# Performance work log

Measured on AMD Instinct MI355X. Metric: run time of the kernel, lower is better.

The kernel has to match this reference:

```python
import jax, jax.numpy as jnp
import numpy as np

N = 200_000   # nodes
E = 6_400_000 # edges (avg degree 32)


def setup_inputs() -> dict:
    key = jax.random.key(0)
    k = jax.random.split(key, 6)
    x = jax.random.normal(k[0], (N, 2), dtype=jnp.float32)
    edge_index = jax.random.randint(k[1], (2, E), 0, N, dtype=jnp.int32)
    # GCNConv(2, 8) and GCNConv(8, 4) parameters (Glorot-ish init, zero bias as in PyG)
    W1 = jax.random.normal(k[2], (2, 8), dtype=jnp.float32) * (1.0 / np.sqrt(2.0))
    b1 = jnp.zeros((8,), dtype=jnp.float32)
    W2 = jax.random.normal(k[3], (8, 4), dtype=jnp.float32) * (1.0 / np.sqrt(8.0))
    b2 = jnp.zeros((4,), dtype=jnp.float32)
    return {"x": x, "edge_index": edge_index, "W1": W1, "b1": b1, "W2": W2, "b2": b2}


def _gcn_conv(x, src, dst, norm, W, b, n):
    # PyG GCNConv: linear transform, normalized gather/scatter-add, bias after aggregation
    h = x @ W                                   # [N, F_out]
    msg = h[src] * norm[:, None]                # gather + edge-wise scale, [E', F_out]
    agg = jax.ops.segment_sum(msg, dst, num_segments=n)  # scatter-add at targets
    return agg + b


def reference(x, edge_index, W1, b1, W2, b2):
    n = x.shape[0]
    # add self-loops (PyG default add_self_loops=True)
    loops = jnp.arange(n, dtype=edge_index.dtype)
    src = jnp.concatenate([edge_index[0], loops])
    dst = jnp.concatenate([edge_index[1], loops])
    # symmetric degree normalization: deg computed at targets with unit edge weights
    deg = jax.ops.segment_sum(jnp.ones_like(src, dtype=x.dtype), dst, num_segments=n)
    deg_inv_sqrt = jnp.where(deg > 0, jax.lax.rsqrt(jnp.maximum(deg, 1.0)), 0.0)
    norm = deg_inv_sqrt[src] * deg_inv_sqrt[dst]  # [E']

    h = jax.nn.relu(_gcn_conv(x, src, dst, norm, W1, b1, n))
    out = _gcn_conv(h, src, dst, norm, W2, b2, n)
    return out
```

## Files before the change

kernel.cpp:

```cpp
#include <hip/hip_runtime.h>


#define EPB   8192
#define PART  2048
#define LPBIT 11
#define SRCB  18
#define BC    4
#define RSTR  2049
#define CAP   70656
#define STCAP 17664


__global__ __launch_bounds__(512) void sortA_kernel(
    const int* __restrict__ src, const int* __restrict__ dst,
    int* __restrict__ cursor, unsigned* __restrict__ packed, int E, int P) {
    __shared__ int cnt[128];
    int tid = threadIdx.x;
    if (tid < 128) cnt[tid] = 0;
    __syncthreads();
    int nv4 = E >> 2;
    int b4 = (blockIdx.x * EPB) >> 2;
    int e4 = min(b4 + (EPB >> 2), nv4);
    const int4* d4 = (const int4*)dst;
    const int4* s4 = (const int4*)src;
    #pragma unroll
    for (int k = 0; k < (EPB >> 2); k += 512) {
        int i = b4 + k + tid;
        if (i < e4) {
            int4 d = d4[i];
            atomicAdd(&cnt[d.x >> LPBIT], 1);
            atomicAdd(&cnt[d.y >> LPBIT], 1);
            atomicAdd(&cnt[d.z >> LPBIT], 1);
            atomicAdd(&cnt[d.w >> LPBIT], 1);
        }
    }
    bool lastblk = (blockIdx.x == gridDim.x - 1);
    if (lastblk) {
        int e = (nv4 << 2) + tid;
        if (e < E) atomicAdd(&cnt[dst[e] >> LPBIT], 1);
    }
    __syncthreads();
    if (tid < P) {
        int c = cnt[tid];
        int base = (c > 0) ? atomicAdd(&cursor[tid], c) : 0;
        cnt[tid] = tid * CAP + base;
    }
    __syncthreads();
    #pragma unroll
    for (int k = 0; k < (EPB >> 2); k += 512) {
        int i = b4 + k + tid;
        if (i < e4) {
            int4 d = d4[i];
            int4 sv = s4[i];
            int p0 = atomicAdd(&cnt[d.x >> LPBIT], 1);
            packed[p0] = ((unsigned)(d.x & (PART - 1)) << SRCB) | (unsigned)sv.x;
            int p1 = atomicAdd(&cnt[d.y >> LPBIT], 1);
            packed[p1] = ((unsigned)(d.y & (PART - 1)) << SRCB) | (unsigned)sv.y;
            int p2 = atomicAdd(&cnt[d.z >> LPBIT], 1);
            packed[p2] = ((unsigned)(d.z & (PART - 1)) << SRCB) | (unsigned)sv.z;
            int p3 = atomicAdd(&cnt[d.w >> LPBIT], 1);
            packed[p3] = ((unsigned)(d.w & (PART - 1)) << SRCB) | (unsigned)sv.w;
        }
    }
    if (lastblk) {
        int e = (nv4 << 2) + tid;
        if (e < E) {
            int d = dst[e];
            int pos = atomicAdd(&cnt[d >> LPBIT], 1);
            packed[pos] = ((unsigned)(d & (PART - 1)) << SRCB) | (unsigned)src[e];
        }
    }
}


__global__ __launch_bounds__(512) void localC_kernel(
    const unsigned* __restrict__ packed, const int* __restrict__ cursor,
    int* __restrict__ runStart, int* __restrict__ srcsorted) {
    __shared__ int hist[PART];
    __shared__ int sdata[512];
    __shared__ unsigned stage[STCAP];
    int tid = threadIdx.x;
    int dp = blockIdx.x >> 2, b = blockIdx.x & (BC - 1);
    int dpbase = dp * CAP;
    int tot = cursor[dp];
    int lo = dpbase + (int)(((long long)tot * b) / BC);
    int hi = dpbase + (int)(((long long)tot * (b + 1)) / BC);
    for (int k = tid; k < PART; k += 512) hist[k] = 0;
    __syncthreads();
    for (int i = lo + tid; i < hi; i += 512)
        atomicAdd(&hist[packed[i] >> SRCB], 1);
    __syncthreads();
    int off = tid * 4;
    int v0 = hist[off], v1 = hist[off + 1], v2 = hist[off + 2], v3 = hist[off + 3];
    int s = v0 + v1 + v2 + v3;
    int x = s;
    sdata[tid] = x;
    __syncthreads();
    for (int o = 1; o < 512; o <<= 1) {
        int t = (tid >= o) ? sdata[tid - o] : 0;
        __syncthreads();
        x += t;
        sdata[tid] = x;
        __syncthreads();
    }
    int run = x - s;
    int* rs = runStart + (size_t)(dp * BC + b) * RSTR;
    int c0 = lo + run, c1 = c0 + v0, c2 = c1 + v1, c3 = c2 + v2;
    rs[off] = c0; rs[off + 1] = c1; rs[off + 2] = c2; rs[off + 3] = c3;
    __syncthreads();
    hist[off] = c0; hist[off + 1] = c1; hist[off + 2] = c2; hist[off + 3] = c3;
    if (tid == 0) rs[PART] = hi;
    __syncthreads();
    int total = hi - lo;
    bool ovf = total > STCAP;
    for (int i = lo + tid; i < hi; i += 512) {
        unsigned w = packed[i];
        int pos = atomicAdd(&hist[w >> SRCB], 1);
        unsigned sv = w & ((1u << SRCB) - 1);
        if (!ovf) stage[pos - lo] = sv;
        else srcsorted[pos] = sv;
    }
    __syncthreads();
    if (!ovf)
        for (int j = tid; j < total; j += 512) srcsorted[lo + j] = (int)stage[j];
}


__global__ __launch_bounds__(512) void dinvg_kernel(
    const int* __restrict__ runStart, const float* __restrict__ x,
    float* __restrict__ dinv, float* __restrict__ g, int n) {
    int i = blockIdx.x * 512 + threadIdx.x;
    if (i >= n) return;
    int dp = i >> LPBIT, ld = i & (PART - 1);
    int deg = 0;
    #pragma unroll
    for (int b = 0; b < BC; b++) {
        const int* rs = runStart + (size_t)(dp * BC + b) * RSTR + ld;
        deg += rs[1] - rs[0];
    }
    float d = rsqrtf((float)deg + 1.0f);
    dinv[i] = d;
    float2 xv = ((const float2*)x)[i];
    ((float2*)g)[i] = make_float2(xv.x * d, xv.y * d);
}

__global__ __launch_bounds__(512) void agg1_kernel(
    const int* __restrict__ runStart, const int* __restrict__ srcsorted,
    const float* __restrict__ g, const float* __restrict__ dinv,
    const float* __restrict__ W1, const float* __restrict__ b1,
    const float* __restrict__ W2, float* __restrict__ hs2, int n) {
    int t = blockIdx.x * 512 + threadIdx.x;
    int i = t >> 2, b = t & 3;
    bool valid = i < n;
    const float2* gp = (const float2*)g;
    float s0 = 0.0f, s1 = 0.0f;
    if (valid) {
        int dp = i >> LPBIT, ld = i & (PART - 1);
        const int* rs = runStart + (size_t)(dp * BC + b) * RSTR + ld;
        int p0 = rs[0], p1 = rs[1];
        int p = p0;
        for (; p + 4 <= p1; p += 4) {
            int a = srcsorted[p], bb = srcsorted[p + 1];
            int c = srcsorted[p + 2], e = srcsorted[p + 3];
            float2 w0 = gp[a], w1 = gp[bb], w2 = gp[c], w3 = gp[e];
            s0 += w0.x + w1.x + w2.x + w3.x;
            s1 += w0.y + w1.y + w2.y + w3.y;
        }
        for (; p < p1; p++) {
            float2 w = gp[srcsorted[p]];
            s0 += w.x;
            s1 += w.y;
        }
    }
    s0 += __shfl_xor(s0, 1); s1 += __shfl_xor(s1, 1);
    s0 += __shfl_xor(s0, 2); s1 += __shfl_xor(s1, 2);
    if (valid && b == 0) {
        float d = dinv[i];
        float2 gi = gp[i];
        s0 = (s0 + gi.x) * d;
        s1 = (s1 + gi.y) * d;
        float h[8];
        #pragma unroll
        for (int f = 0; f < 8; f++)
            h[f] = fmaxf(s0 * W1[f] + s1 * W1[8 + f] + b1[f], 0.0f);
        float oc[4];
        #pragma unroll
        for (int k = 0; k < 4; k++) {
            float a = 0.0f;
            #pragma unroll
            for (int f = 0; f < 8; f++) a += h[f] * W2[4 * f + k];
            oc[k] = a * d;
        }
        float4 o;
        o.x = oc[0]; o.y = oc[1]; o.z = oc[2]; o.w = oc[3];
        *(float4*)(hs2 + 4 * (size_t)i) = o;
    }
}

__global__ __launch_bounds__(512) void agg2_kernel(
    const int* __restrict__ runStart, const int* __restrict__ srcsorted,
    const float* __restrict__ hs2, const float* __restrict__ dinv,
    const float* __restrict__ b2, float* __restrict__ out, int n) {
    int t = blockIdx.x * 512 + threadIdx.x;
    int i = t >> 2, b = t & 3;
    bool valid = i < n;
    const float4* hp = (const float4*)hs2;
    float s0 = 0.0f, s1 = 0.0f, s2 = 0.0f, s3 = 0.0f;
    if (valid) {
        int dp = i >> LPBIT, ld = i & (PART - 1);
        const int* rs = runStart + (size_t)(dp * BC + b) * RSTR + ld;
        int p0 = rs[0], p1 = rs[1];
        int p = p0;
        for (; p + 4 <= p1; p += 4) {
            int a = srcsorted[p], bb = srcsorted[p + 1];
            int c = srcsorted[p + 2], e = srcsorted[p + 3];
            float4 w0 = hp[a], w1 = hp[bb], w2 = hp[c], w3 = hp[e];
            s0 += w0.x + w1.x + w2.x + w3.x;
            s1 += w0.y + w1.y + w2.y + w3.y;
            s2 += w0.z + w1.z + w2.z + w3.z;
            s3 += w0.w + w1.w + w2.w + w3.w;
        }
        for (; p < p1; p++) {
            float4 w = hp[srcsorted[p]];
            s0 += w.x; s1 += w.y; s2 += w.z; s3 += w.w;
        }
    }
    s0 += __shfl_xor(s0, 1); s1 += __shfl_xor(s1, 1);
    s2 += __shfl_xor(s2, 1); s3 += __shfl_xor(s3, 1);
    s0 += __shfl_xor(s0, 2); s1 += __shfl_xor(s1, 2);
    s2 += __shfl_xor(s2, 2); s3 += __shfl_xor(s3, 2);
    if (valid && b == 0) {
        float d = dinv[i];
        float4 hi2 = hp[i];
        float4 o;
        o.x = d * (s0 + hi2.x) + b2[0];
        o.y = d * (s1 + hi2.y) + b2[1];
        o.z = d * (s2 + hi2.z) + b2[2];
        o.w = d * (s3 + hi2.w) + b2[3];
        *(float4*)(out + 4 * (size_t)i) = o;
    }
}

extern "C" void kernel_launch(void* const* d_in, const int* in_sizes, int n_in,
                              void* d_out, int out_size, void* d_ws, size_t ws_size,
                              hipStream_t stream) {
    const float* x   = (const float*)d_in[0];
    const int*   ei  = (const int*)d_in[1];
    const float* W1  = (const float*)d_in[2];
    const float* b1  = (const float*)d_in[3];
    const float* W2  = (const float*)d_in[4];
    const float* b2  = (const float*)d_in[5];
    float* out = (float*)d_out;

    const int n = in_sizes[0] / 2;
    const int E = in_sizes[1] / 2;
    const int* src = ei;
    const int* dst = ei + E;

    const int P  = (n + PART - 1) >> LPBIT;
    const int B1 = (E + EPB - 1) / EPB;

    int* ws = (int*)d_ws;
    int* cursor = ws;
    int* runStart = ws + 128;
    size_t rssz = (((size_t)P * BC * RSTR) + 3) & ~(size_t)3;
    unsigned* packed = (unsigned*)(runStart + rssz);
    int* srcsorted = (int*)(packed + (size_t)P * CAP);
    size_t nd = (size_t)P << LPBIT;
    float* dinv = (float*)packed;
    float* g    = dinv + nd;
    float* hs2  = g + 2 * nd;

    hipMemsetAsync(cursor, 0, 128 * sizeof(int), stream);

    const int gN  = (n + 511) / 512;
    const int gN4 = (4 * n + 511) / 512;

    sortA_kernel <<<B1, 512, 0, stream>>>(src, dst, cursor, packed, E, P);
    localC_kernel<<<P * BC, 512, 0, stream>>>(packed, cursor, runStart, srcsorted);
    dinvg_kernel <<<gN, 512, 0, stream>>>(runStart, x, dinv, g, n);
    agg1_kernel  <<<gN4, 512, 0, stream>>>(runStart, srcsorted, g, dinv, W1, b1, W2, hs2, n);
    agg2_kernel  <<<gN4, 512, 0, stream>>>(runStart, srcsorted, hs2, dinv, b2, out, n);
}
```

Before: 252.5 us.

## Use per-wave partition counters in sort and split each node's edges over eight lanes

```diff
diff --git a/kernel.cpp b/kernel.cpp
--- a/kernel.cpp
+++ b/kernel.cpp
@@ -5,60 +5,70 @@
 #define PART  2048
 #define LPBIT 11
 #define SRCB  18
-#define BC    4
+#define BC    8
 #define RSTR  2049
-#define CAP   70656
-#define STCAP 17664
+#define CAP   69632
+#define STCAP 8704
+#define WV    8
 
 
 __global__ __launch_bounds__(512) void sortA_kernel(
     const int* __restrict__ src, const int* __restrict__ dst,
     int* __restrict__ cursor, unsigned* __restrict__ packed, int E, int P) {
-    __shared__ int cnt[128];
+    __shared__ int cnt[WV * 128];
+    __shared__ int wcur[WV * 128];
     int tid = threadIdx.x;
-    if (tid < 128) cnt[tid] = 0;
+    int wid = tid >> 6;
+    for (int k = tid; k < WV * 128; k += 512) cnt[k] = 0;
     __syncthreads();
     int nv4 = E >> 2;
     int b4 = (blockIdx.x * EPB) >> 2;
     int e4 = min(b4 + (EPB >> 2), nv4);
     const int4* d4 = (const int4*)dst;
     const int4* s4 = (const int4*)src;
+    int* mycnt = cnt + wid * 128;
     #pragma unroll
     for (int k = 0; k < (EPB >> 2); k += 512) {
         int i = b4 + k + tid;
         if (i < e4) {
             int4 d = d4[i];
-            atomicAdd(&cnt[d.x >> LPBIT], 1);
-            atomicAdd(&cnt[d.y >> LPBIT], 1);
-            atomicAdd(&cnt[d.z >> LPBIT], 1);
-            atomicAdd(&cnt[d.w >> LPBIT], 1);
+            atomicAdd(&mycnt[d.x >> LPBIT], 1);
+            atomicAdd(&mycnt[d.y >> LPBIT], 1);
+            atomicAdd(&mycnt[d.z >> LPBIT], 1);
+            atomicAdd(&mycnt[d.w >> LPBIT], 1);
         }
     }
     bool lastblk = (blockIdx.x == gridDim.x - 1);
     if (lastblk) {
         int e = (nv4 << 2) + tid;
-        if (e < E) atomicAdd(&cnt[dst[e] >> LPBIT], 1);
-    }
-    __syncthreads();
-    if (tid < P) {
-        int c = cnt[tid];
-        int base = (c > 0) ? atomicAdd(&cursor[tid], c) : 0;
-        cnt[tid] = tid * CAP + base;
-    }
-    __syncthreads();
+        if (e < E) atomicAdd(&mycnt[dst[e] >> LPBIT], 1);
+    }
+    __syncthreads();
+    if (tid < 128) {
+        int c[WV];
+        int tot = 0;
+        #pragma unroll
+        for (int w = 0; w < WV; w++) { c[w] = cnt[w * 128 + tid]; tot += c[w]; }
+        int base = (tot > 0) ? atomicAdd(&cursor[tid], tot) : 0;
+        int run = tid * CAP + base;
+        #pragma unroll
+        for (int w = 0; w < WV; w++) { wcur[w * 128 + tid] = run; run += c[w]; }
+    }
+    __syncthreads();
+    int* mycur = wcur + wid * 128;
     #pragma unroll
     for (int k = 0; k < (EPB >> 2); k += 512) {
         int i = b4 + k + tid;
         if (i < e4) {
             int4 d = d4[i];
             int4 sv = s4[i];
-            int p0 = atomicAdd(&cnt[d.x >> LPBIT], 1);
+            int p0 = atomicAdd(&mycur[d.x >> LPBIT], 1);
             packed[p0] = ((unsigned)(d.x & (PART - 1)) << SRCB) | (unsigned)sv.x;
-            int p1 = atomicAdd(&cnt[d.y >> LPBIT], 1);
+            int p1 = atomicAdd(&mycur[d.y >> LPBIT], 1);
             packed[p1] = ((unsigned)(d.y & (PART - 1)) << SRCB) | (unsigned)sv.y;
-            int p2 = atomicAdd(&cnt[d.z >> LPBIT], 1);
+            int p2 = atomicAdd(&mycur[d.z >> LPBIT], 1);
             packed[p2] = ((unsigned)(d.z & (PART - 1)) << SRCB) | (unsigned)sv.z;
-            int p3 = atomicAdd(&cnt[d.w >> LPBIT], 1);
+            int p3 = atomicAdd(&mycur[d.w >> LPBIT], 1);
             packed[p3] = ((unsigned)(d.w & (PART - 1)) << SRCB) | (unsigned)sv.w;
         }
     }
@@ -66,7 +76,7 @@
         int e = (nv4 << 2) + tid;
         if (e < E) {
             int d = dst[e];
-            int pos = atomicAdd(&cnt[d >> LPBIT], 1);
+            int pos = atomicAdd(&mycur[d >> LPBIT], 1);
             packed[pos] = ((unsigned)(d & (PART - 1)) << SRCB) | (unsigned)src[e];
         }
     }
@@ -80,7 +90,7 @@
     __shared__ int sdata[512];
     __shared__ unsigned stage[STCAP];
     int tid = threadIdx.x;
-    int dp = blockIdx.x >> 2, b = blockIdx.x & (BC - 1);
+    int dp = blockIdx.x >> 3, b = blockIdx.x & (BC - 1);
     int dpbase = dp * CAP;
     int tot = cursor[dp];
     int lo = dpbase + (int)(((long long)tot * b) / BC);
@@ -129,19 +139,25 @@
 __global__ __launch_bounds__(512) void dinvg_kernel(
     const int* __restrict__ runStart, const float* __restrict__ x,
     float* __restrict__ dinv, float* __restrict__ g, int n) {
-    int i = blockIdx.x * 512 + threadIdx.x;
-    if (i >= n) return;
-    int dp = i >> LPBIT, ld = i & (PART - 1);
+    int t = blockIdx.x * 512 + threadIdx.x;
+    int lane = threadIdx.x & 63;
+    int node = (t >> 6) * 8 + (lane & 7);
+    int b = lane >> 3;
     int deg = 0;
-    #pragma unroll
-    for (int b = 0; b < BC; b++) {
+    if (node < n) {
+        int dp = node >> LPBIT, ld = node & (PART - 1);
         const int* rs = runStart + (size_t)(dp * BC + b) * RSTR + ld;
-        deg += rs[1] - rs[0];
-    }
-    float d = rsqrtf((float)deg + 1.0f);
-    dinv[i] = d;
-    float2 xv = ((const float2*)x)[i];
-    ((float2*)g)[i] = make_float2(xv.x * d, xv.y * d);
+        deg = rs[1] - rs[0];
+    }
+    deg += __shfl_xor(deg, 8);
+    deg += __shfl_xor(deg, 16);
+    deg += __shfl_xor(deg, 32);
+    if (node < n && b == 0) {
+        float d = rsqrtf((float)deg + 1.0f);
+        dinv[node] = d;
+        float2 xv = ((const float2*)x)[node];
+        ((float2*)g)[node] = make_float2(xv.x * d, xv.y * d);
+    }
 }
 
 __global__ __launch_bounds__(512) void agg1_kernel(
@@ -150,12 +166,13 @@
     const float* __restrict__ W1, const float* __restrict__ b1,
     const float* __restrict__ W2, float* __restrict__ hs2, int n) {
     int t = blockIdx.x * 512 + threadIdx.x;
-    int i = t >> 2, b = t & 3;
-    bool valid = i < n;
+    int lane = threadIdx.x & 63;
+    int node = (t >> 6) * 8 + (lane & 7);
+    int b = lane >> 3;
     const float2* gp = (const float2*)g;
     float s0 = 0.0f, s1 = 0.0f;
-    if (valid) {
-        int dp = i >> LPBIT, ld = i & (PART - 1);
+    if (node < n) {
+        int dp = node >> LPBIT, ld = node & (PART - 1);
         const int* rs = runStart + (size_t)(dp * BC + b) * RSTR + ld;
         int p0 = rs[0], p1 = rs[1];
         int p = p0;
@@ -172,11 +189,12 @@
             s1 += w.y;
         }
     }
-    s0 += __shfl_xor(s0, 1); s1 += __shfl_xor(s1, 1);
-    s0 += __shfl_xor(s0, 2); s1 += __shfl_xor(s1, 2);
-    if (valid && b == 0) {
-        float d = dinv[i];
-        float2 gi = gp[i];
+    s0 += __shfl_xor(s0, 8);  s1 += __shfl_xor(s1, 8);
+    s0 += __shfl_xor(s0, 16); s1 += __shfl_xor(s1, 16);
+    s0 += __shfl_xor(s0, 32); s1 += __shfl_xor(s1, 32);
+    if (node < n && b == 0) {
+        float d = dinv[node];
+        float2 gi = gp[node];
         s0 = (s0 + gi.x) * d;
         s1 = (s1 + gi.y) * d;
         float h[8];
@@ -193,7 +211,7 @@
         }
         float4 o;
         o.x = oc[0]; o.y = oc[1]; o.z = oc[2]; o.w = oc[3];
-        *(float4*)(hs2 + 4 * (size_t)i) = o;
+        *(float4*)(hs2 + 4 * (size_t)node) = o;
     }
 }
 
@@ -202,12 +220,13 @@
     const float* __restrict__ hs2, const float* __restrict__ dinv,
     const float* __restrict__ b2, float* __restrict__ out, int n) {
     int t = blockIdx.x * 512 + threadIdx.x;
-    int i = t >> 2, b = t & 3;
-    bool valid = i < n;
+    int lane = threadIdx.x & 63;
+    int node = (t >> 6) * 8 + (lane & 7);
+    int b = lane >> 3;
     const float4* hp = (const float4*)hs2;
     float s0 = 0.0f, s1 = 0.0f, s2 = 0.0f, s3 = 0.0f;
-    if (valid) {
-        int dp = i >> LPBIT, ld = i & (PART - 1);
+    if (node < n) {
+        int dp = node >> LPBIT, ld = node & (PART - 1);
         const int* rs = runStart + (size_t)(dp * BC + b) * RSTR + ld;
         int p0 = rs[0], p1 = rs[1];
         int p = p0;
@@ -225,19 +244,21 @@
             s0 += w.x; s1 += w.y; s2 += w.z; s3 += w.w;
         }
     }
-    s0 += __shfl_xor(s0, 1); s1 += __shfl_xor(s1, 1);
-    s2 += __shfl_xor(s2, 1); s3 += __shfl_xor(s3, 1);
-    s0 += __shfl_xor(s0, 2); s1 += __shfl_xor(s1, 2);
-    s2 += __shfl_xor(s2, 2); s3 += __shfl_xor(s3, 2);
-    if (valid && b == 0) {
-        float d = dinv[i];
-        float4 hi2 = hp[i];
+    s0 += __shfl_xor(s0, 8);  s1 += __shfl_xor(s1, 8);
+    s2 += __shfl_xor(s2, 8);  s3 += __shfl_xor(s3, 8);
+    s0 += __shfl_xor(s0, 16); s1 += __shfl_xor(s1, 16);
+    s2 += __shfl_xor(s2, 16); s3 += __shfl_xor(s3, 16);
+    s0 += __shfl_xor(s0, 32); s1 += __shfl_xor(s1, 32);
+    s2 += __shfl_xor(s2, 32); s3 += __shfl_xor(s3, 32);
+    if (node < n && b == 0) {
+        float d = dinv[node];
+        float4 hi2 = hp[node];
         float4 o;
         o.x = d * (s0 + hi2.x) + b2[0];
         o.y = d * (s1 + hi2.y) + b2[1];
         o.z = d * (s2 + hi2.z) + b2[2];
         o.w = d * (s3 + hi2.w) + b2[3];
-        *(float4*)(out + 4 * (size_t)i) = o;
+        *(float4*)(out + 4 * (size_t)node) = o;
     }
 }
 
@@ -273,12 +294,11 @@
 
     hipMemsetAsync(cursor, 0, 128 * sizeof(int), stream);
 
-    const int gN  = (n + 511) / 512;
-    const int gN4 = (4 * n + 511) / 512;
+    const int gB = (n + 63) / 64;
 
     sortA_kernel <<<B1, 512, 0, stream>>>(src, dst, cursor, packed, E, P);
     localC_kernel<<<P * BC, 512, 0, stream>>>(packed, cursor, runStart, srcsorted);
-    dinvg_kernel <<<gN, 512, 0, stream>>>(runStart, x, dinv, g, n);
-    agg1_kernel  <<<gN4, 512, 0, stream>>>(runStart, srcsorted, g, dinv, W1, b1, W2, hs2, n);
-    agg2_kernel  <<<gN4, 512, 0, stream>>>(runStart, srcsorted, hs2, dinv, b2, out, n);
-}
+    dinvg_kernel <<<gB, 512, 0, stream>>>(runStart, x, dinv, g, n);
+    agg1_kernel  <<<gB, 512, 0, stream>>>(runStart, srcsorted, g, dinv, W1, b1, W2, hs2, n);
+    agg2_kernel  <<<gB, 512, 0, stream>>>(runStart, srcsorted, hs2, dinv, b2, out, n);
+}
```

New measurement: 254.2 us. Within noise of the previous version (+0.7%).

## Cache edges in registers in sortA and use one thread per node in aggregation

Applied to the files above, without the earlier changes.

```diff
diff --git a/kernel.cpp b/kernel.cpp
--- a/kernel.cpp
+++ b/kernel.cpp
@@ -7,8 +7,8 @@
 #define SRCB  18
 #define BC    4
 #define RSTR  2049
-#define CAP   70656
-#define STCAP 17664
+#define CAP   69632
+#define STCAP 17408
 
 
 __global__ __launch_bounds__(512) void sortA_kernel(
@@ -20,55 +20,60 @@
     __syncthreads();
     int nv4 = E >> 2;
     int b4 = (blockIdx.x * EPB) >> 2;
-    int e4 = min(b4 + (EPB >> 2), nv4);
     const int4* d4 = (const int4*)dst;
     const int4* s4 = (const int4*)src;
-    #pragma unroll
-    for (int k = 0; k < (EPB >> 2); k += 512) {
-        int i = b4 + k + tid;
-        if (i < e4) {
-            int4 d = d4[i];
-            atomicAdd(&cnt[d.x >> LPBIT], 1);
-            atomicAdd(&cnt[d.y >> LPBIT], 1);
-            atomicAdd(&cnt[d.z >> LPBIT], 1);
-            atomicAdd(&cnt[d.w >> LPBIT], 1);
+    int4 dv[4], sv[4];
+    bool inb[4];
+    #pragma unroll
+    for (int k = 0; k < 4; k++) {
+        int i = b4 + k * 512 + tid;
+        inb[k] = (i < nv4);
+        if (inb[k]) {
+            dv[k] = d4[i];
+            sv[k] = s4[i];
+            atomicAdd(&cnt[dv[k].x >> LPBIT], 1);
+            atomicAdd(&cnt[dv[k].y >> LPBIT], 1);
+            atomicAdd(&cnt[dv[k].z >> LPBIT], 1);
+            atomicAdd(&cnt[dv[k].w >> LPBIT], 1);
         }
     }
     bool lastblk = (blockIdx.x == gridDim.x - 1);
+    int tsrc = 0, tdst = 0;
+    bool tin = false;
     if (lastblk) {
         int e = (nv4 << 2) + tid;
-        if (e < E) atomicAdd(&cnt[dst[e] >> LPBIT], 1);
-    }
-    __syncthreads();
-    if (tid < P) {
+        tin = (e < E);
+        if (tin) {
+            tdst = dst[e];
+            tsrc = src[e];
+            atomicAdd(&cnt[tdst >> LPBIT], 1);
+        }
+    }
+    __syncthreads();
+    if (tid < 128) {
         int c = cnt[tid];
         int base = (c > 0) ? atomicAdd(&cursor[tid], c) : 0;
         cnt[tid] = tid * CAP + base;
     }
     __syncthreads();
     #pragma unroll
-    for (int k = 0; k < (EPB >> 2); k += 512) {
-        int i = b4 + k + tid;
-        if (i < e4) {
-            int4 d = d4[i];
-            int4 sv = s4[i];
+    for (int k = 0; k < 4; k++) {
+        if (inb[k]) {
+            int4 d = dv[k];
+            int4 s = sv[k];
             int p0 = atomicAdd(&cnt[d.x >> LPBIT], 1);
-            packed[p0] = ((unsigned)(d.x & (PART - 1)) << SRCB) | (unsigned)sv.x;
+            packed[p0] = ((unsigned)(d.x & (PART - 1)) << SRCB) | (unsigned)s.x;
             int p1 = atomicAdd(&cnt[d.y >> LPBIT], 1);
-            packed[p1] = ((unsigned)(d.y & (PART - 1)) << SRCB) | (unsigned)sv.y;
+            packed[p1] = ((unsigned)(d.y & (PART - 1)) << SRCB) | (unsigned)s.y;
             int p2 = atomicAdd(&cnt[d.z >> LPBIT], 1);
-            packed[p2] = ((unsigned)(d.z & (PART - 1)) << SRCB) | (unsigned)sv.z;
+            packed[p2] = ((unsigned)(d.z & (PART - 1)) << SRCB) | (unsigned)s.z;
             int p3 = atomicAdd(&cnt[d.w >> LPBIT], 1);
-            packed[p3] = ((unsigned)(d.w & (PART - 1)) << SRCB) | (unsigned)sv.w;
-        }
-    }
-    if (lastblk) {
-        int e = (nv4 << 2) + tid;
-        if (e < E) {
-            int d = dst[e];
-            int pos = atomicAdd(&cnt[d >> LPBIT], 1);
-            packed[pos] = ((unsigned)(d & (PART - 1)) << SRCB) | (unsigned)src[e];
-        }
+            packed[p3] = ((unsigned)(d.w & (PART - 1)) << SRCB) | (unsigned)s.w;
+        }
+    }
+    if (tin) {
+        int pos = atomicAdd(&cnt[tdst >> LPBIT], 1);
+        packed[pos] = ((unsigned)(tdst & (PART - 1)) << SRCB) | (unsigned)tsrc;
     }
 }
 
@@ -149,13 +154,13 @@
     const float* __restrict__ g, const float* __restrict__ dinv,
     const float* __restrict__ W1, const float* __restrict__ b1,
     const float* __restrict__ W2, float* __restrict__ hs2, int n) {
-    int t = blockIdx.x * 512 + threadIdx.x;
-    int i = t >> 2, b = t & 3;
-    bool valid = i < n;
+    int i = blockIdx.x * 512 + threadIdx.x;
+    if (i >= n) return;
+    int dp = i >> LPBIT, ld = i & (PART - 1);
     const float2* gp = (const float2*)g;
     float s0 = 0.0f, s1 = 0.0f;
-    if (valid) {
-        int dp = i >> LPBIT, ld = i & (PART - 1);
+    #pragma unroll
+    for (int b = 0; b < BC; b++) {
         const int* rs = runStart + (size_t)(dp * BC + b) * RSTR + ld;
         int p0 = rs[0], p1 = rs[1];
         int p = p0;
@@ -172,42 +177,38 @@
             s1 += w.y;
         }
     }
-    s0 += __shfl_xor(s0, 1); s1 += __shfl_xor(s1, 1);
-    s0 += __shfl_xor(s0, 2); s1 += __shfl_xor(s1, 2);
-    if (valid && b == 0) {
-        float d = dinv[i];
-        float2 gi = gp[i];
-        s0 = (s0 + gi.x) * d;
-        s1 = (s1 + gi.y) * d;
-        float h[8];
+    float d = dinv[i];
+    float2 gi = gp[i];
+    s0 = (s0 + gi.x) * d;
+    s1 = (s1 + gi.y) * d;
+    float h[8];
+    #pragma unroll
+    for (int f = 0; f < 8; f++)
+        h[f] = fmaxf(s0 * W1[f] + s1 * W1[8 + f] + b1[f], 0.0f);
+    float oc[4];
+    #pragma unroll
+    for (int k = 0; k < 4; k++) {
+        float a = 0.0f;
         #pragma unroll
-        for (int f = 0; f < 8; f++)
-            h[f] = fmaxf(s0 * W1[f] + s1 * W1[8 + f] + b1[f], 0.0f);
-        float oc[4];
-        #pragma unroll
-        for (int k = 0; k < 4; k++) {
-            float a = 0.0f;
-            #pragma unroll
-            for (int f = 0; f < 8; f++) a += h[f] * W2[4 * f + k];
-            oc[k] = a * d;
-        }
-        float4 o;
-        o.x = oc[0]; o.y = oc[1]; o.z = oc[2]; o.w = oc[3];
-        *(float4*)(hs2 + 4 * (size_t)i) = o;
-    }
+        for (int f = 0; f < 8; f++) a += h[f] * W2[4 * f + k];
+        oc[k] = a * d;
+    }
+    float4 o;
+    o.x = oc[0]; o.y = oc[1]; o.z = oc[2]; o.w = oc[3];
+    *(float4*)(hs2 + 4 * (size_t)i) = o;
 }
 
 __global__ __launch_bounds__(512) void agg2_kernel(
     const int* __restrict__ runStart, const int* __restrict__ srcsorted,
     const float* __restrict__ hs2, const float* __restrict__ dinv,
     const float* __restrict__ b2, float* __restrict__ out, int n) {
-    int t = blockIdx.x * 512 + threadIdx.x;
-    int i = t >> 2, b = t & 3;
-    bool valid = i < n;
+    int i = blockIdx.x * 512 + threadIdx.x;
+    if (i >= n) return;
+    int dp = i >> LPBIT, ld = i & (PART - 1);
     const float4* hp = (const float4*)hs2;
     float s0 = 0.0f, s1 = 0.0f, s2 = 0.0f, s3 = 0.0f;
-    if (valid) {
-        int dp = i >> LPBIT, ld = i & (PART - 1);
+    #pragma unroll
+    for (int b = 0; b < BC; b++) {
         const int* rs = runStart + (size_t)(dp * BC + b) * RSTR + ld;
         int p0 = rs[0], p1 = rs[1];
         int p = p0;
@@ -225,20 +226,14 @@
             s0 += w.x; s1 += w.y; s2 += w.z; s3 += w.w;
         }
     }
-    s0 += __shfl_xor(s0, 1); s1 += __shfl_xor(s1, 1);
-    s2 += __shfl_xor(s2, 1); s3 += __shfl_xor(s3, 1);
-    s0 += __shfl_xor(s0, 2); s1 += __shfl_xor(s1, 2);
-    s2 += __shfl_xor(s2, 2); s3 += __shfl_xor(s3, 2);
-    if (valid && b == 0) {
-        float d = dinv[i];
-        float4 hi2 = hp[i];
-        float4 o;
-        o.x = d * (s0 + hi2.x) + b2[0];
-        o.y = d * (s1 + hi2.y) + b2[1];
-        o.z = d * (s2 + hi2.z) + b2[2];
-        o.w = d * (s3 + hi2.w) + b2[3];
-        *(float4*)(out + 4 * (size_t)i) = o;
-    }
+    float d = dinv[i];
+    float4 hi2 = hp[i];
+    float4 o;
+    o.x = d * (s0 + hi2.x) + b2[0];
+    o.y = d * (s1 + hi2.y) + b2[1];
+    o.z = d * (s2 + hi2.z) + b2[2];
+    o.w = d * (s3 + hi2.w) + b2[3];
+    *(float4*)(out + 4 * (size_t)i) = o;
 }
 
 extern "C" void kernel_launch(void* const* d_in, const int* in_sizes, int n_in,
@@ -273,12 +268,11 @@
 
     hipMemsetAsync(cursor, 0, 128 * sizeof(int), stream);
 
-    const int gN  = (n + 511) / 512;
-    const int gN4 = (4 * n + 511) / 512;
+    const int gN = (n + 511) / 512;
 
     sortA_kernel <<<B1, 512, 0, stream>>>(src, dst, cursor, packed, E, P);
     localC_kernel<<<P * BC, 512, 0, stream>>>(packed, cursor, runStart, srcsorted);
     dinvg_kernel <<<gN, 512, 0, stream>>>(runStart, x, dinv, g, n);
-    agg1_kernel  <<<gN4, 512, 0, stream>>>(runStart, srcsorted, g, dinv, W1, b1, W2, hs2, n);
-    agg2_kernel  <<<gN4, 512, 0, stream>>>(runStart, srcsorted, hs2, dinv, b2, out, n);
-}
+    agg1_kernel  <<<gN, 512, 0, stream>>>(runStart, srcsorted, g, dinv, W1, b1, W2, hs2, n);
+    agg2_kernel  <<<gN, 512, 0, stream>>>(runStart, srcsorted, hs2, dinv, b2, out, n);
+}
```

After: 247.6 us. Within noise of the previous version (-1.9%).
